# Performance work log

Measured on AMD Instinct MI355X. Metric: run time of the kernel, lower is better.

The kernel has to match this reference:

```python
import jax, jax.numpy as jnp
import numpy as np
from functools import partial

VOCAB = 32000
EMBED = 512
HIDDEN = 1024
NUM_LAYERS = 2
REP_PENALTY = 1.2
BATCH, SEQ = 64, 128


def _lstm_layer(xs, w_ih, w_hh, b_ih, b_hh):
    """PyTorch-convention LSTM layer. xs: [B,T,D_in] -> hs: [B,T,H].
    Gate order i,f,g,o; weights [4H, D_in]/[4H, H]."""
    B = xs.shape[0]
    H = w_hh.shape[1]
    # precompute input projections for all timesteps: [B,T,4H]
    x_proj = jnp.einsum('btd,gd->btg', xs, w_ih) + b_ih + b_hh

    def step(carry, xp):
        h, c = carry
        gates = xp + h @ w_hh.T  # [B,4H]
        i, f, g, o = jnp.split(gates, 4, axis=-1)
        i = jax.nn.sigmoid(i)
        f = jax.nn.sigmoid(f)
        g = jnp.tanh(g)
        o = jax.nn.sigmoid(o)
        c = f * c + i * g
        h = o * jnp.tanh(c)
        return (h, c), h

    h0 = jnp.zeros((B, H), xs.dtype)
    c0 = jnp.zeros((B, H), xs.dtype)
    _, hs = jax.lax.scan(step, (h0, c0), x_proj.transpose(1, 0, 2))  # [T,B,H]
    return hs.transpose(1, 0, 2)


def setup_inputs() -> dict:
    key = jax.random.key(0)
    ks = jax.random.split(key, 16)
    s_emb = 1.0  # nn.Embedding default init ~ N(0,1)
    x = jax.random.randint(ks[0], (BATCH, SEQ), 0, VOCAB, dtype=jnp.int32)
    emb = jax.random.normal(ks[1], (VOCAB, EMBED), jnp.float32) * s_emb

    def lstm_params(k, d_in):
        k1, k2, k3, k4 = jax.random.split(k, 4)
        s = 1.0 / np.sqrt(HIDDEN)
        return (
            jax.random.uniform(k1, (4 * HIDDEN, d_in), jnp.float32, -s, s),
            jax.random.uniform(k2, (4 * HIDDEN, HIDDEN), jnp.float32, -s, s),
            jax.random.uniform(k3, (4 * HIDDEN,), jnp.float32, -s, s),
            jax.random.uniform(k4, (4 * HIDDEN,), jnp.float32, -s, s),
        )

    w_ih0, w_hh0, b_ih0, b_hh0 = lstm_params(ks[2], EMBED)
    w_ih1, w_hh1, b_ih1, b_hh1 = lstm_params(ks[3], HIDDEN)
    s_fc = 1.0 / np.sqrt(HIDDEN)
    fc_w = jax.random.uniform(ks[4], (VOCAB, HIDDEN), jnp.float32, -s_fc, s_fc)
    fc_b = jax.random.uniform(ks[5], (VOCAB,), jnp.float32, -s_fc, s_fc)
    return {
        'x': x, 'emb': emb,
        'w_ih0': w_ih0, 'w_hh0': w_hh0, 'b_ih0': b_ih0, 'b_hh0': b_hh0,
        'w_ih1': w_ih1, 'w_hh1': w_hh1, 'b_ih1': b_ih1, 'b_hh1': b_hh1,
        'fc_w': fc_w, 'fc_b': fc_b,
    }


def reference(x, emb, w_ih0, w_hh0, b_ih0, b_hh0,
              w_ih1, w_hh1, b_ih1, b_hh1, fc_w, fc_b):
    h = emb[x]                                          # [B,S,E] embedding lookup
    h = _lstm_layer(h, w_ih0, w_hh0, b_ih0, b_hh0)      # [B,S,H]
    h = _lstm_layer(h, w_ih1, w_hh1, b_ih1, b_hh1)      # [B,S,H]
    last = h[:, -1, :]                                  # [B,H]
    out = last @ fc_w.T + fc_b                          # [B,V]
    # repetition penalty: each occurrence of token t in row i divides out[i,t]
    # by the penalty once => out[i,t] /= penalty**count(t in x[i]).
    B = x.shape[0]
    rows = jnp.broadcast_to(jnp.arange(B)[:, None], x.shape)
    counts = jnp.zeros((B, VOCAB), out.dtype).at[rows, x].add(1.0)
    out = out / jnp.power(jnp.asarray(REP_PENALTY, out.dtype), counts)
    return out
```

## Files before the change

kernel.cpp:

```cpp
#include <hip/hip_runtime.h>
#include <hip/hip_bf16.h>
#include <stdint.h>

#define NB 64
#define NT 128
#define NE 512
#define NH 1024
#define NV 32000
#define NM (NB*NT)

#define NWG 256
#define NTH 512
#define FLAG_STRIDE 32u

#define HSLOT_B (NB*NH*2u)
#define WS_FLAGS   0u
#define WS_FLAG_B  (NWG*FLAG_STRIDE*4u)
#define WS_H0      WS_FLAG_B
#define WS_H1      (WS_H0 + 129u*HSLOT_B)
#define WS_CNT     (WS_H1 + 129u*HSLOT_B)
#define WS_XS0     (WS_CNT + 4u*NB*NV)
#define WS_NEEDED  (WS_XS0 + 2u*NM*NE)

typedef __attribute__((ext_vector_type(8))) short bf16x8;
typedef __attribute__((ext_vector_type(4))) float f32x4;

__device__ __forceinline__ unsigned short f2bf(float f) {
  unsigned u = __float_as_uint(f);
  u += 0x7FFFu + ((u >> 16) & 1u);
  return (unsigned short)(u >> 16);
}
__device__ __forceinline__ float sigmoidf_(float x) {
  return 1.0f / (1.0f + expf(-x));
}
__device__ __forceinline__ bf16x8 pack8(float4 a, float4 b) {
  bf16x8 v;
  v[0]=(short)f2bf(a.x); v[1]=(short)f2bf(a.y); v[2]=(short)f2bf(a.z); v[3]=(short)f2bf(a.w);
  v[4]=(short)f2bf(b.x); v[5]=(short)f2bf(b.y); v[6]=(short)f2bf(b.z); v[7]=(short)f2bf(b.w);
  return v;
}

__device__ __forceinline__ void gbar_light(unsigned* flags, unsigned n) {
  __syncthreads();
  if (threadIdx.x == 0)
    __hip_atomic_store(&flags[(unsigned)blockIdx.x * FLAG_STRIDE], n,
                       __ATOMIC_RELAXED, __HIP_MEMORY_SCOPE_AGENT);
  if (threadIdx.x < NWG) {
    while (__hip_atomic_load(&flags[(unsigned)threadIdx.x * FLAG_STRIDE],
                             __ATOMIC_RELAXED, __HIP_MEMORY_SCOPE_AGENT) < n)
      __builtin_amdgcn_s_sleep(8);
  }
  __syncthreads();
}

#define MFMA(a,b,c) __builtin_amdgcn_mfma_f32_16x16x32_bf16((a),(b),(c),0,0,0)

__global__ void __launch_bounds__(NTH, 2)
lstm_all(const int* __restrict__ x, const float* __restrict__ emb,
         const float* __restrict__ w_ih0, const float* __restrict__ w_hh0,
         const float* __restrict__ b_ih0, const float* __restrict__ b_hh0,
         const float* __restrict__ w_ih1, const float* __restrict__ w_hh1,
         const float* __restrict__ b_ih1, const float* __restrict__ b_hh1,
         const float* __restrict__ fc_w, const float* __restrict__ fc_b,
         float* __restrict__ out, unsigned char* __restrict__ wsb)
{
  __shared__ unsigned short sWih1[32*64*8];
  __shared__ unsigned short sWih0[16*64*8];
  __shared__ float sG0[NB][16], sG1a[NB][16], sG1b[NB][16], sGih[NB][16];
  __shared__ float sB0[16], sB1[16];
  __shared__ alignas(8) unsigned short sH0[NB][4], sH1[NB][4];

  const int wg  = blockIdx.x;
  const int tid = threadIdx.x;
  const int wave = tid >> 6, lane = tid & 63;
  const int lr = lane & 15, lq = lane >> 4;

  unsigned* flags = (unsigned*)(wsb + WS_FLAGS);
  unsigned short* hist0 = (unsigned short*)(wsb + WS_H0);
  unsigned short* hist1 = (unsigned short*)(wsb + WS_H1);
  unsigned* counts = (unsigned*)(wsb + WS_CNT);
  unsigned short* xs0 = (unsigned short*)(wsb + WS_XS0);

  const int gr = (lr >> 2)*NH + wg*4 + (lr & 3);

  const unsigned kkw = (unsigned)wg >> 3, lqw = ((unsigned)wg >> 1) & 3, j0 = ((unsigned)wg & 1)*4;
  const size_t pubOff = ((size_t)((lane>>4)*32 + kkw)*64 + lqw*16 + (lane&15))*8 + j0;

  bf16x8 breg[32];
  {
    const float* wsrc = (wave < 4 ? w_hh0 : w_hh1) + (size_t)gr*NH + lq*8;
    #pragma unroll
    for (int kk = 0; kk < 32; ++kk)
      breg[kk] = pack8(*(const float4*)(wsrc + kk*32), *(const float4*)(wsrc + kk*32 + 4));
  }

  for (int i = wg*NTH + tid; i < NM*(NE/8); i += NWG*NTH) {
    int m = i >> 6;
    int e8 = (i & 63) << 3;
    int t = m >> 6, b = m & 63;
    int tok = x[b*NT + t];
    const float* s = emb + (size_t)tok*NE + e8;
    union { bf16x8 v8; unsigned long long u[2]; } u;
    u.v8 = pack8(*(const float4*)s, *(const float4*)(s + 4));
    int mblk = m >> 4, lrm = m & 15;
    int kk = e8 >> 5, lqm = (e8 >> 3) & 3;
    size_t elem = ((size_t)(mblk*16 + kk)*64 + lqm*16 + lrm) * 8;
    unsigned long long* dst = (unsigned long long*)(xs0 + elem);
    __hip_atomic_store(dst,   u.u[0], __ATOMIC_RELAXED, __HIP_MEMORY_SCOPE_AGENT);
    __hip_atomic_store(dst+1, u.u[1], __ATOMIC_RELAXED, __HIP_MEMORY_SCOPE_AGENT);
  }

  for (int i = tid; i < 32*64; i += NTH) {
    int kk = i >> 6, l = i & 63;
    int glr = l & 15, glq = l >> 4;
    int ggr = (glr >> 2)*NH + wg*4 + (glr & 3);
    const float* p = w_ih1 + (size_t)ggr*NH + kk*32 + glq*8;
    ((bf16x8*)sWih1)[i] = pack8(*(const float4*)p, *(const float4*)(p + 4));
  }
  for (int i = tid; i < 16*64; i += NTH) {
    int kk = i >> 6, l = i & 63;
    int glr = l & 15, glq = l >> 4;
    int ggr = (glr >> 2)*NH + wg*4 + (glr & 3);
    const float* p = w_ih0 + (size_t)ggr*NE + kk*32 + glq*8;
    ((bf16x8*)sWih0)[i] = pack8(*(const float4*)p, *(const float4*)(p + 4));
  }
  if (tid < 16) {
    int g2 = (tid >> 2)*NH + wg*4 + (tid & 3);
    sB0[tid] = b_ih0[g2] + b_hh0[g2];
    sB1[tid] = b_ih1[g2] + b_hh1[g2];
  }
  {
    int i = wg*NTH + tid;
    if (i < NB*NT) {
      int b = i >> 7;
      atomicAdd(&counts[(size_t)b*NV + x[i]], 1u);
    }
  }
  unsigned bar = 1;
  gbar_light(flags, bar);

  float c_reg = 0.f;
  const int cb = (tid & 255) >> 2, cu = tid & 3;
  for (int t = 0; t <= NT; ++t) {
    if (wave < 4) {
      const unsigned short* A = hist0 + (size_t)t*(NB*NH) + (size_t)(wave*2048 + lane)*8;
      f32x4 a0 = {0.f,0.f,0.f,0.f}, a1 = {0.f,0.f,0.f,0.f};
      #pragma unroll
      for (int kk = 0; kk < 32; ++kk) {
        bf16x8 af = *(const bf16x8*)(A + kk*512);
        a0 = MFMA(af, breg[kk], a0);
        a1 = MFMA(af, ((const bf16x8*)sWih1)[kk*64 + lane], a1);
      }
      #pragma unroll
      for (int r = 0; r < 4; ++r) {
        sG0 [wave*16 + lq*4 + r][lr] = a0[r];
        sG1a[wave*16 + lq*4 + r][lr] = a1[r];
      }
    } else {
      if (t >= 1) {
        const unsigned short* A = hist1 + (size_t)(t-1)*(NB*NH) + (size_t)((wave-4)*2048 + lane)*8;
        f32x4 a2 = {0.f,0.f,0.f,0.f};
        #pragma unroll
        for (int kk = 0; kk < 32; ++kk)
          a2 = MFMA(*(const bf16x8*)(A + kk*512), breg[kk], a2);
        #pragma unroll
        for (int r = 0; r < 4; ++r) sG1b[(wave-4)*16 + lq*4 + r][lr] = a2[r];
      }
      if (t < NT) {
        const unsigned short* A = xs0 + ((size_t)(t*4 + (wave-4))*1024 + lane)*8;
        f32x4 ai = {0.f,0.f,0.f,0.f};
        #pragma unroll
        for (int kk = 0; kk < 16; ++kk)
          ai = MFMA(*(const bf16x8*)(A + kk*512), ((const bf16x8*)sWih0)[kk*64 + lane], ai);
        #pragma unroll
        for (int r = 0; r < 4; ++r) sGih[(wave-4)*16 + lq*4 + r][lr] = ai[r];
      }
    }
    __syncthreads();
    if (tid < 256) {
      if (t < NT) {
        float gi = sG0[cb][cu]    + sGih[cb][cu]    + sB0[cu];
        float gf = sG0[cb][4+cu]  + sGih[cb][4+cu]  + sB0[4+cu];
        float gg = sG0[cb][8+cu]  + sGih[cb][8+cu]  + sB0[8+cu];
        float go = sG0[cb][12+cu] + sGih[cb][12+cu] + sB0[12+cu];
        float ii = sigmoidf_(gi), ff = sigmoidf_(gf), g = tanhf(gg), oo = sigmoidf_(go);
        c_reg = ff*c_reg + ii*g;
        sH0[cb][cu] = f2bf(oo * tanhf(c_reg));
      }
    } else {
      if (t >= 1) {
        float gi = sG1a[cb][cu]    + sG1b[cb][cu]    + sB1[cu];
        float gf = sG1a[cb][4+cu]  + sG1b[cb][4+cu]  + sB1[4+cu];
        float gg = sG1a[cb][8+cu]  + sG1b[cb][8+cu]  + sB1[8+cu];
        float go = sG1a[cb][12+cu] + sG1b[cb][12+cu] + sB1[12+cu];
        float ii = sigmoidf_(gi), ff = sigmoidf_(gf), g = tanhf(gg), oo = sigmoidf_(go);
        c_reg = ff*c_reg + ii*g;
        sH1[cb][cu] = f2bf(oo * tanhf(c_reg));
      }
    }
    __syncthreads();
    if (wave == 0 && t < NT) {
      unsigned long long v = *(const unsigned long long*)&sH0[lane][0];
      __hip_atomic_store((unsigned long long*)(hist0 + (size_t)(t+1)*(NB*NH) + pubOff),
                         v, __ATOMIC_RELAXED, __HIP_MEMORY_SCOPE_AGENT);
    }
    if (wave == 1 && t >= 1) {
      unsigned long long v = *(const unsigned long long*)&sH1[lane][0];
      __hip_atomic_store((unsigned long long*)(hist1 + (size_t)t*(NB*NH) + pubOff),
                         v, __ATOMIC_RELAXED, __HIP_MEMORY_SCOPE_AGENT);
    }
    gbar_light(flags, ++bar);
  }

  {
    const unsigned short* ab = hist1 + (size_t)128*(NB*NH) + (size_t)lane*8;
    int tile = wg*8 + wave;
    if (tile < NV/16) {
      int c0 = tile*16;
      const float* wb = fc_w + (size_t)(c0 + lr)*NH + lq*8;
      f32x4 acc[4] = {{0.f,0.f,0.f,0.f},{0.f,0.f,0.f,0.f},{0.f,0.f,0.f,0.f},{0.f,0.f,0.f,0.f}};
      #pragma unroll 4
      for (int kk = 0; kk < 32; ++kk) {
        bf16x8 bfv = pack8(*(const float4*)(wb + kk*32), *(const float4*)(wb + kk*32 + 4));
        #pragma unroll
        for (int mt = 0; mt < 4; ++mt) {
          bf16x8 af = *(const bf16x8*)(ab + (size_t)(mt*32 + kk)*512);
          acc[mt] = MFMA(af, bfv, acc[mt]);
        }
      }
      int c = c0 + lr;
      float fb = fc_b[c];
      #pragma unroll
      for (int mt = 0; mt < 4; ++mt) {
        #pragma unroll
        for (int r = 0; r < 4; ++r) {
          int b = mt*16 + lq*4 + r;
          unsigned cnt = counts[(size_t)b*NV + c];
          float v = (acc[mt][r] + fb) * exp2f(-0.26303440583379378f * (float)cnt);
          out[(size_t)b*NV + c] = v;
        }
      }
    }
  }
}

extern "C" void kernel_launch(void* const* d_in, const int* in_sizes, int n_in,
                              void* d_out, int out_size, void* d_ws, size_t ws_size,
                              hipStream_t stream) {
  const int*   x     = (const int*)  d_in[0];
  const float* emb   = (const float*)d_in[1];
  const float* w_ih0 = (const float*)d_in[2];
  const float* w_hh0 = (const float*)d_in[3];
  const float* b_ih0 = (const float*)d_in[4];
  const float* b_hh0 = (const float*)d_in[5];
  const float* w_ih1 = (const float*)d_in[6];
  const float* w_hh1 = (const float*)d_in[7];
  const float* b_ih1 = (const float*)d_in[8];
  const float* b_hh1 = (const float*)d_in[9];
  const float* fc_w  = (const float*)d_in[10];
  const float* fc_b  = (const float*)d_in[11];
  if (ws_size < WS_NEEDED) return;
  unsigned char* ws = (unsigned char*)d_ws;
  hipMemsetAsync(ws + WS_FLAGS, 0, WS_FLAG_B, stream);
  hipMemsetAsync(ws + WS_H0, 0, HSLOT_B, stream);
  hipMemsetAsync(ws + WS_H1, 0, HSLOT_B, stream);
  hipMemsetAsync(ws + WS_CNT, 0, 4u*NB*NV, stream);
  hipLaunchKernelGGL(lstm_all, dim3(NWG), dim3(NTH), 0, stream,
                     x, emb, w_ih0, w_hh0, b_ih0, b_hh0,
                     w_ih1, w_hh1, b_ih1, b_hh1, fc_w, fc_b,
                     (float*)d_out, (unsigned char*)d_ws);
}
```

Before: 998.9 us.

## Decouple LSTM layer waves with per-wave flags and LDS counters instead of grid barriers

Replaces the lock-step per-timestep grid barrier with separate global flag arrays for layer 0 and layer 1. Each wave polls only the 64 workgroups whose outputs it consumes, and waves inside a workgroup coordinate through LDS atomic counters. Layer-0 waves now also compute the input projection, and a 4-deep LDS ring buffers the layer-1 input-projection partials, so layer 1 can trail layer 0 in a wavefront pipeline instead of sharing one barrier. The goal is to remove full-grid barrier latency and idle time on the serial recurrence. In exchange the hand-rolled memory ordering (relaxed stores, manual waitcnt and fence macros, spin loops) is harder to reason about and could deadlock or race.

```diff
diff --git a/kernel.cpp b/kernel.cpp
--- a/kernel.cpp
+++ b/kernel.cpp
@@ -8,15 +8,17 @@
 #define NH 1024
 #define NV 32000
 #define NM (NB*NT)
+#define NBNH (NB*NH)
 
 #define NWG 256
 #define NTH 512
 #define FLAG_STRIDE 32u
 
 #define HSLOT_B (NB*NH*2u)
-#define WS_FLAGS   0u
-#define WS_FLAG_B  (NWG*FLAG_STRIDE*4u)
-#define WS_H0      WS_FLAG_B
+#define WS_FLAGS_S 0u
+#define WS_FLAGS_A (32u*1024u)
+#define WS_FLAGS_B (64u*1024u)
+#define WS_H0      (96u*1024u)
 #define WS_H1      (WS_H0 + 129u*HSLOT_B)
 #define WS_CNT     (WS_H1 + 129u*HSLOT_B)
 #define WS_XS0     (WS_CNT + 4u*NB*NV)
@@ -24,6 +26,13 @@
 
 typedef __attribute__((ext_vector_type(8))) short bf16x8;
 typedef __attribute__((ext_vector_type(4))) float f32x4;
+
+#define SCOPE_WG  __HIP_MEMORY_SCOPE_WORKGROUP
+#define SCOPE_AG  __HIP_MEMORY_SCOPE_AGENT
+
+#define FENCE() do { asm volatile("" ::: "memory"); __builtin_amdgcn_sched_barrier(0); } while (0)
+#define LGKM0() do { asm volatile("s_waitcnt lgkmcnt(0)" ::: "memory"); __builtin_amdgcn_sched_barrier(0); } while (0)
+#define VM0()   do { asm volatile("s_waitcnt vmcnt(0)" ::: "memory"); __builtin_amdgcn_sched_barrier(0); } while (0)
 
 __device__ __forceinline__ unsigned short f2bf(float f) {
   unsigned u = __float_as_uint(f);
@@ -43,11 +52,9 @@
 __device__ __forceinline__ void gbar_light(unsigned* flags, unsigned n) {
   __syncthreads();
   if (threadIdx.x == 0)
-    __hip_atomic_store(&flags[(unsigned)blockIdx.x * FLAG_STRIDE], n,
-                       __ATOMIC_RELAXED, __HIP_MEMORY_SCOPE_AGENT);
+    __hip_atomic_store(&flags[(unsigned)blockIdx.x * FLAG_STRIDE], n, __ATOMIC_RELAXED, SCOPE_AG);
   if (threadIdx.x < NWG) {
-    while (__hip_atomic_load(&flags[(unsigned)threadIdx.x * FLAG_STRIDE],
-                             __ATOMIC_RELAXED, __HIP_MEMORY_SCOPE_AGENT) < n)
+    while (__hip_atomic_load(&flags[(unsigned)threadIdx.x * FLAG_STRIDE], __ATOMIC_RELAXED, SCOPE_AG) < n)
       __builtin_amdgcn_s_sleep(8);
   }
   __syncthreads();
@@ -66,16 +73,20 @@
 {
   __shared__ unsigned short sWih1[32*64*8];
   __shared__ unsigned short sWih0[16*64*8];
-  __shared__ float sG0[NB][16], sG1a[NB][16], sG1b[NB][16], sGih[NB][16];
+  __shared__ float sG0[NB][16], sGih[NB][16], sG1b[NB][16];
+  __shared__ float ringP[4][NB][16];
   __shared__ float sB0[16], sB1[16];
   __shared__ alignas(8) unsigned short sH0[NB][4], sH1[NB][4];
+  __shared__ unsigned ldsCnt[12];
 
   const int wg  = blockIdx.x;
   const int tid = threadIdx.x;
   const int wave = tid >> 6, lane = tid & 63;
   const int lr = lane & 15, lq = lane >> 4;
 
-  unsigned* flags = (unsigned*)(wsb + WS_FLAGS);
+  unsigned* flagsS = (unsigned*)(wsb + WS_FLAGS_S);
+  unsigned* flagsA = (unsigned*)(wsb + WS_FLAGS_A);
+  unsigned* flagsB = (unsigned*)(wsb + WS_FLAGS_B);
   unsigned short* hist0 = (unsigned short*)(wsb + WS_H0);
   unsigned short* hist1 = (unsigned short*)(wsb + WS_H1);
   unsigned* counts = (unsigned*)(wsb + WS_CNT);
@@ -84,7 +95,8 @@
   const int gr = (lr >> 2)*NH + wg*4 + (lr & 3);
 
   const unsigned kkw = (unsigned)wg >> 3, lqw = ((unsigned)wg >> 1) & 3, j0 = ((unsigned)wg & 1)*4;
-  const size_t pubOff = ((size_t)((lane>>4)*32 + kkw)*64 + lqw*16 + (lane&15))*8 + j0;
+
+  if (tid < 12) ldsCnt[tid] = 0;
 
   bf16x8 breg[32];
   {
@@ -106,8 +118,8 @@
     int kk = e8 >> 5, lqm = (e8 >> 3) & 3;
     size_t elem = ((size_t)(mblk*16 + kk)*64 + lqm*16 + lrm) * 8;
     unsigned long long* dst = (unsigned long long*)(xs0 + elem);
-    __hip_atomic_store(dst,   u.u[0], __ATOMIC_RELAXED, __HIP_MEMORY_SCOPE_AGENT);
-    __hip_atomic_store(dst+1, u.u[1], __ATOMIC_RELAXED, __HIP_MEMORY_SCOPE_AGENT);
+    __hip_atomic_store(dst,   u.u[0], __ATOMIC_RELAXED, SCOPE_AG);
+    __hip_atomic_store(dst+1, u.u[1], __ATOMIC_RELAXED, SCOPE_AG);
   }
 
   for (int i = tid; i < 32*64; i += NTH) {
@@ -136,84 +148,150 @@
       atomicAdd(&counts[(size_t)b*NV + x[i]], 1u);
     }
   }
-  unsigned bar = 1;
-  gbar_light(flags, bar);
-
-  float c_reg = 0.f;
-  const int cb = (tid & 255) >> 2, cu = tid & 3;
-  for (int t = 0; t <= NT; ++t) {
-    if (wave < 4) {
-      const unsigned short* A = hist0 + (size_t)t*(NB*NH) + (size_t)(wave*2048 + lane)*8;
-      f32x4 a0 = {0.f,0.f,0.f,0.f}, a1 = {0.f,0.f,0.f,0.f};
-      #pragma unroll
-      for (int kk = 0; kk < 32; ++kk) {
-        bf16x8 af = *(const bf16x8*)(A + kk*512);
-        a0 = MFMA(af, breg[kk], a0);
-        a1 = MFMA(af, ((const bf16x8*)sWih1)[kk*64 + lane], a1);
-      }
-      #pragma unroll
-      for (int r = 0; r < 4; ++r) {
-        sG0 [wave*16 + lq*4 + r][lr] = a0[r];
-        sG1a[wave*16 + lq*4 + r][lr] = a1[r];
-      }
-    } else {
-      if (t >= 1) {
-        const unsigned short* A = hist1 + (size_t)(t-1)*(NB*NH) + (size_t)((wave-4)*2048 + lane)*8;
-        f32x4 a2 = {0.f,0.f,0.f,0.f};
+  gbar_light(flagsS, 1);
+
+  const int cbl = lane >> 2, cu = lane & 3;
+
+  if (wave < 4) {
+    const int w = wave;
+    const size_t pubOffW = ((size_t)(w*32 + kkw)*64 + lqw*16 + lane)*8 + j0;
+    float c0 = 0.f;
+    for (int t = 0; t <= NT; ++t) {
+      while (__hip_atomic_load(&flagsA[(unsigned)(w*64 + lane)*FLAG_STRIDE],
+                               __ATOMIC_RELAXED, SCOPE_AG) < (unsigned)t)
+        __builtin_amdgcn_s_sleep(1);
+      if (lane == 0) {
+        __hip_atomic_fetch_add(&ldsCnt[10], 1u, __ATOMIC_ACQ_REL, SCOPE_WG);
+        while (__hip_atomic_load(&ldsCnt[10], __ATOMIC_ACQUIRE, SCOPE_WG) < 4u*(unsigned)(t+1)) {}
+      }
+      FENCE();
+      if (t >= 4) {
+        if (lane == 0)
+          while (__hip_atomic_load(&ldsCnt[4+w], __ATOMIC_ACQUIRE, SCOPE_WG) < (unsigned)(t-3)) {}
+        FENCE();
+      }
+      const unsigned short* A = hist0 + (size_t)t*NBNH + (size_t)(w*2048 + lane)*8;
+      f32x4 a0 = {0.f,0.f,0.f,0.f}, a1 = {0.f,0.f,0.f,0.f}, ai = {0.f,0.f,0.f,0.f};
+      if (t < NT) {
+        #pragma unroll
+        for (int kk = 0; kk < 32; ++kk) {
+          bf16x8 af = *(const bf16x8*)(A + kk*512);
+          a0 = MFMA(af, breg[kk], a0);
+          a1 = MFMA(af, ((const bf16x8*)sWih1)[kk*64 + lane], a1);
+        }
+        const unsigned short* X = xs0 + ((size_t)(t*4 + w)*1024 + lane)*8;
+        #pragma unroll
+        for (int kk = 0; kk < 16; ++kk)
+          ai = MFMA(*(const bf16x8*)(X + kk*512), ((const bf16x8*)sWih0)[kk*64 + lane], ai);
+      } else {
         #pragma unroll
         for (int kk = 0; kk < 32; ++kk)
-          a2 = MFMA(*(const bf16x8*)(A + kk*512), breg[kk], a2);
-        #pragma unroll
-        for (int r = 0; r < 4; ++r) sG1b[(wave-4)*16 + lq*4 + r][lr] = a2[r];
+          a1 = MFMA(*(const bf16x8*)(A + kk*512), ((const bf16x8*)sWih1)[kk*64 + lane], a1);
+      }
+      {
+        int rs = t & 3;
+        #pragma unroll
+        for (int r = 0; r < 4; ++r) ringP[rs][w*16 + lq*4 + r][lr] = a1[r];
       }
       if (t < NT) {
-        const unsigned short* A = xs0 + ((size_t)(t*4 + (wave-4))*1024 + lane)*8;
-        f32x4 ai = {0.f,0.f,0.f,0.f};
-        #pragma unroll
-        for (int kk = 0; kk < 16; ++kk)
-          ai = MFMA(*(const bf16x8*)(A + kk*512), ((const bf16x8*)sWih0)[kk*64 + lane], ai);
-        #pragma unroll
-        for (int r = 0; r < 4; ++r) sGih[(wave-4)*16 + lq*4 + r][lr] = ai[r];
-      }
-    }
-    __syncthreads();
-    if (tid < 256) {
+        #pragma unroll
+        for (int r = 0; r < 4; ++r) {
+          sG0 [w*16 + lq*4 + r][lr] = a0[r];
+          sGih[w*16 + lq*4 + r][lr] = ai[r];
+        }
+      }
+      LGKM0();
+      if (lane == 0)
+        __hip_atomic_fetch_add(&ldsCnt[w], 1u, __ATOMIC_RELEASE, SCOPE_WG);
       if (t < NT) {
+        int cb = w*16 + cbl;
         float gi = sG0[cb][cu]    + sGih[cb][cu]    + sB0[cu];
         float gf = sG0[cb][4+cu]  + sGih[cb][4+cu]  + sB0[4+cu];
         float gg = sG0[cb][8+cu]  + sGih[cb][8+cu]  + sB0[8+cu];
         float go = sG0[cb][12+cu] + sGih[cb][12+cu] + sB0[12+cu];
         float ii = sigmoidf_(gi), ff = sigmoidf_(gf), g = tanhf(gg), oo = sigmoidf_(go);
-        c_reg = ff*c_reg + ii*g;
-        sH0[cb][cu] = f2bf(oo * tanhf(c_reg));
-      }
-    } else {
-      if (t >= 1) {
-        float gi = sG1a[cb][cu]    + sG1b[cb][cu]    + sB1[cu];
-        float gf = sG1a[cb][4+cu]  + sG1b[cb][4+cu]  + sB1[4+cu];
-        float gg = sG1a[cb][8+cu]  + sG1b[cb][8+cu]  + sB1[8+cu];
-        float go = sG1a[cb][12+cu] + sG1b[cb][12+cu] + sB1[12+cu];
+        c0 = ff*c0 + ii*g;
+        sH0[cb][cu] = f2bf(oo * tanhf(c0));
+        LGKM0();
+        if (lane < 16) {
+          unsigned long long v = *(const unsigned long long*)&sH0[w*16 + lane][0];
+          __hip_atomic_store((unsigned long long*)(hist0 + (size_t)(t+1)*NBNH + pubOffW),
+                             v, __ATOMIC_RELAXED, SCOPE_AG);
+        }
+        VM0();
+        if (lane == 0)
+          __hip_atomic_fetch_add(&ldsCnt[8], 1u, __ATOMIC_RELEASE, SCOPE_WG);
+        if (w == 0 && lane == 0) {
+          while (__hip_atomic_load(&ldsCnt[8], __ATOMIC_ACQUIRE, SCOPE_WG) < 4u*(unsigned)(t+1)) {}
+          __hip_atomic_store(&flagsA[(unsigned)wg*FLAG_STRIDE], (unsigned)(t+1),
+                             __ATOMIC_RELAXED, SCOPE_AG);
+        }
+      }
+    }
+  } else {
+    const int w1 = wave - 4;
+    const size_t pubOffW = ((size_t)(w1*32 + kkw)*64 + lqw*16 + lane)*8 + j0;
+    float c1 = 0.f;
+    for (int s = 0; s < NT; ++s) {
+      while (__hip_atomic_load(&flagsB[(unsigned)(w1*64 + lane)*FLAG_STRIDE],
+                               __ATOMIC_RELAXED, SCOPE_AG) < (unsigned)s)
+        __builtin_amdgcn_s_sleep(1);
+      if (lane == 0) {
+        __hip_atomic_fetch_add(&ldsCnt[11], 1u, __ATOMIC_ACQ_REL, SCOPE_WG);
+        while (__hip_atomic_load(&ldsCnt[11], __ATOMIC_ACQUIRE, SCOPE_WG) < 4u*(unsigned)(s+1)) {}
+      }
+      FENCE();
+      if (lane == 0)
+        while (__hip_atomic_load(&ldsCnt[w1], __ATOMIC_ACQUIRE, SCOPE_WG) < (unsigned)(s+2)) {}
+      FENCE();
+      const unsigned short* A = hist1 + (size_t)s*NBNH + (size_t)(w1*2048 + lane)*8;
+      f32x4 a2 = {0.f,0.f,0.f,0.f};
+      #pragma unroll
+      for (int kk = 0; kk < 32; ++kk)
+        a2 = MFMA(*(const bf16x8*)(A + kk*512), breg[kk], a2);
+      #pragma unroll
+      for (int r = 0; r < 4; ++r) sG1b[w1*16 + lq*4 + r][lr] = a2[r];
+      LGKM0();
+      {
+        int cb = w1*16 + cbl;
+        int rs = (s+1) & 3;
+        float gi = ringP[rs][cb][cu]    + sG1b[cb][cu]    + sB1[cu];
+        float gf = ringP[rs][cb][4+cu]  + sG1b[cb][4+cu]  + sB1[4+cu];
+        float gg = ringP[rs][cb][8+cu]  + sG1b[cb][8+cu]  + sB1[8+cu];
+        float go = ringP[rs][cb][12+cu] + sG1b[cb][12+cu] + sB1[12+cu];
         float ii = sigmoidf_(gi), ff = sigmoidf_(gf), g = tanhf(gg), oo = sigmoidf_(go);
-        c_reg = ff*c_reg + ii*g;
-        sH1[cb][cu] = f2bf(oo * tanhf(c_reg));
+        c1 = ff*c1 + ii*g;
+        sH1[cb][cu] = f2bf(oo * tanhf(c1));
+      }
+      if (lane == 0)
+        __hip_atomic_fetch_add(&ldsCnt[4+w1], 1u, __ATOMIC_RELEASE, SCOPE_WG);
+      LGKM0();
+      if (lane < 16) {
+        unsigned long long v = *(const unsigned long long*)&sH1[w1*16 + lane][0];
+        __hip_atomic_store((unsigned long long*)(hist1 + (size_t)(s+1)*NBNH + pubOffW),
+                           v, __ATOMIC_RELAXED, SCOPE_AG);
+      }
+      VM0();
+      if (lane == 0)
+        __hip_atomic_fetch_add(&ldsCnt[9], 1u, __ATOMIC_RELEASE, SCOPE_WG);
+      if (w1 == 0 && lane == 0) {
+        while (__hip_atomic_load(&ldsCnt[9], __ATOMIC_ACQUIRE, SCOPE_WG) < 4u*(unsigned)(s+1)) {}
+        __hip_atomic_store(&flagsB[(unsigned)wg*FLAG_STRIDE], (unsigned)(s+1),
+                           __ATOMIC_RELAXED, SCOPE_AG);
       }
     }
-    __syncthreads();
-    if (wave == 0 && t < NT) {
-      unsigned long long v = *(const unsigned long long*)&sH0[lane][0];
-      __hip_atomic_store((unsigned long long*)(hist0 + (size_t)(t+1)*(NB*NH) + pubOff),
-                         v, __ATOMIC_RELAXED, __HIP_MEMORY_SCOPE_AGENT);
-    }
-    if (wave == 1 && t >= 1) {
-      unsigned long long v = *(const unsigned long long*)&sH1[lane][0];
-      __hip_atomic_store((unsigned long long*)(hist1 + (size_t)t*(NB*NH) + pubOff),
-                         v, __ATOMIC_RELAXED, __HIP_MEMORY_SCOPE_AGENT);
-    }
-    gbar_light(flags, ++bar);
-  }
+  }
+
+  __syncthreads();
+  if (tid < NWG) {
+    while (__hip_atomic_load(&flagsB[(unsigned)tid*FLAG_STRIDE], __ATOMIC_RELAXED, SCOPE_AG)
+           < (unsigned)NT)
+      __builtin_amdgcn_s_sleep(4);
+  }
+  __syncthreads();
 
   {
-    const unsigned short* ab = hist1 + (size_t)128*(NB*NH) + (size_t)lane*8;
+    const unsigned short* ab = hist1 + (size_t)128*NBNH + (size_t)lane*8;
     int tile = wg*8 + wave;
     if (tile < NV/16) {
       int c0 = tile*16;
@@ -261,7 +339,7 @@
   const float* fc_b  = (const float*)d_in[11];
   if (ws_size < WS_NEEDED) return;
   unsigned char* ws = (unsigned char*)d_ws;
-  hipMemsetAsync(ws + WS_FLAGS, 0, WS_FLAG_B, stream);
+  hipMemsetAsync(ws, 0, WS_H0, stream);
   hipMemsetAsync(ws + WS_H0, 0, HSLOT_B, stream);
   hipMemsetAsync(ws + WS_H1, 0, HSLOT_B, stream);
   hipMemsetAsync(ws + WS_CNT, 0, 4u*NB*NV, stream);
```

Result: slower. 1.343 ms (+34.4%).

## Replace per-step global barrier with split per-layer flag counters

Applied to the files above, without the earlier changes.

Replaces the single grid-wide barrier per timestep with separate layer-0 and layer-1 progress flags. Each workgroup waits only on the flags its next step depends on, and each wave publishes its own h slice with a workgroup-local counter that raises the flag once all four waves are done. This removes one block-wide sync and lets the two layers drift apart instead of marching in lockstep. The cost is more spin-polling traffic and subtle memory-ordering requirements around relaxed stores and waitcnt-based fences.

```diff
diff --git a/kernel.cpp b/kernel.cpp
--- a/kernel.cpp
+++ b/kernel.cpp
@@ -8,15 +8,17 @@
 #define NH 1024
 #define NV 32000
 #define NM (NB*NT)
+#define NBNH (NB*NH)
 
 #define NWG 256
 #define NTH 512
 #define FLAG_STRIDE 32u
 
 #define HSLOT_B (NB*NH*2u)
-#define WS_FLAGS   0u
-#define WS_FLAG_B  (NWG*FLAG_STRIDE*4u)
-#define WS_H0      WS_FLAG_B
+#define WS_FLAGS_S 0u
+#define WS_FLAGS_A (32u*1024u)
+#define WS_FLAGS_B (64u*1024u)
+#define WS_H0      (96u*1024u)
 #define WS_H1      (WS_H0 + 129u*HSLOT_B)
 #define WS_CNT     (WS_H1 + 129u*HSLOT_B)
 #define WS_XS0     (WS_CNT + 4u*NB*NV)
@@ -24,6 +26,12 @@
 
 typedef __attribute__((ext_vector_type(8))) short bf16x8;
 typedef __attribute__((ext_vector_type(4))) float f32x4;
+
+#define SCOPE_WG  __HIP_MEMORY_SCOPE_WORKGROUP
+#define SCOPE_AG  __HIP_MEMORY_SCOPE_AGENT
+
+#define LGKM0() do { asm volatile("s_waitcnt lgkmcnt(0)" ::: "memory"); __builtin_amdgcn_sched_barrier(0); } while (0)
+#define VM0()   do { asm volatile("s_waitcnt vmcnt(0)" ::: "memory"); __builtin_amdgcn_sched_barrier(0); } while (0)
 
 __device__ __forceinline__ unsigned short f2bf(float f) {
   unsigned u = __float_as_uint(f);
@@ -43,11 +51,9 @@
 __device__ __forceinline__ void gbar_light(unsigned* flags, unsigned n) {
   __syncthreads();
   if (threadIdx.x == 0)
-    __hip_atomic_store(&flags[(unsigned)blockIdx.x * FLAG_STRIDE], n,
-                       __ATOMIC_RELAXED, __HIP_MEMORY_SCOPE_AGENT);
+    __hip_atomic_store(&flags[(unsigned)blockIdx.x * FLAG_STRIDE], n, __ATOMIC_RELAXED, SCOPE_AG);
   if (threadIdx.x < NWG) {
-    while (__hip_atomic_load(&flags[(unsigned)threadIdx.x * FLAG_STRIDE],
-                             __ATOMIC_RELAXED, __HIP_MEMORY_SCOPE_AGENT) < n)
+    while (__hip_atomic_load(&flags[(unsigned)threadIdx.x * FLAG_STRIDE], __ATOMIC_RELAXED, SCOPE_AG) < n)
       __builtin_amdgcn_s_sleep(8);
   }
   __syncthreads();
@@ -66,16 +72,19 @@
 {
   __shared__ unsigned short sWih1[32*64*8];
   __shared__ unsigned short sWih0[16*64*8];
-  __shared__ float sG0[NB][16], sG1a[NB][16], sG1b[NB][16], sGih[NB][16];
+  __shared__ float sG0[NB][16], sGih[NB][16], sG1a[NB][16], sG1b[NB][16];
   __shared__ float sB0[16], sB1[16];
   __shared__ alignas(8) unsigned short sH0[NB][4], sH1[NB][4];
+  __shared__ unsigned cntA, cntB;
 
   const int wg  = blockIdx.x;
   const int tid = threadIdx.x;
   const int wave = tid >> 6, lane = tid & 63;
   const int lr = lane & 15, lq = lane >> 4;
 
-  unsigned* flags = (unsigned*)(wsb + WS_FLAGS);
+  unsigned* flagsS = (unsigned*)(wsb + WS_FLAGS_S);
+  unsigned* flagsA = (unsigned*)(wsb + WS_FLAGS_A);
+  unsigned* flagsB = (unsigned*)(wsb + WS_FLAGS_B);
   unsigned short* hist0 = (unsigned short*)(wsb + WS_H0);
   unsigned short* hist1 = (unsigned short*)(wsb + WS_H1);
   unsigned* counts = (unsigned*)(wsb + WS_CNT);
@@ -84,7 +93,10 @@
   const int gr = (lr >> 2)*NH + wg*4 + (lr & 3);
 
   const unsigned kkw = (unsigned)wg >> 3, lqw = ((unsigned)wg >> 1) & 3, j0 = ((unsigned)wg & 1)*4;
-  const size_t pubOff = ((size_t)((lane>>4)*32 + kkw)*64 + lqw*16 + (lane&15))*8 + j0;
+  const unsigned rbw = (unsigned)(wave & 3);
+  const size_t pubOff = ((size_t)(rbw*32 + kkw)*64 + lqw*16 + lane)*8 + j0;
+
+  if (tid == 0) { cntA = 0; cntB = 0; }
 
   bf16x8 breg[32];
   {
@@ -106,8 +118,8 @@
     int kk = e8 >> 5, lqm = (e8 >> 3) & 3;
     size_t elem = ((size_t)(mblk*16 + kk)*64 + lqm*16 + lrm) * 8;
     unsigned long long* dst = (unsigned long long*)(xs0 + elem);
-    __hip_atomic_store(dst,   u.u[0], __ATOMIC_RELAXED, __HIP_MEMORY_SCOPE_AGENT);
-    __hip_atomic_store(dst+1, u.u[1], __ATOMIC_RELAXED, __HIP_MEMORY_SCOPE_AGENT);
+    __hip_atomic_store(dst,   u.u[0], __ATOMIC_RELAXED, SCOPE_AG);
+    __hip_atomic_store(dst+1, u.u[1], __ATOMIC_RELAXED, SCOPE_AG);
   }
 
   for (int i = tid; i < 32*64; i += NTH) {
@@ -136,29 +148,57 @@
       atomicAdd(&counts[(size_t)b*NV + x[i]], 1u);
     }
   }
-  unsigned bar = 1;
-  gbar_light(flags, bar);
+  gbar_light(flagsS, 1);
 
   float c_reg = 0.f;
   const int cb = (tid & 255) >> 2, cu = tid & 3;
   for (int t = 0; t <= NT; ++t) {
+    if (tid < NWG) {
+      while (__hip_atomic_load(&flagsA[(unsigned)tid * FLAG_STRIDE],
+                               __ATOMIC_RELAXED, SCOPE_AG) < (unsigned)t)
+        __builtin_amdgcn_s_sleep(2);
+    } else {
+      unsigned need = (t > 0) ? (unsigned)(t - 1) : 0u;
+      while (__hip_atomic_load(&flagsB[(unsigned)(tid - NWG) * FLAG_STRIDE],
+                               __ATOMIC_RELAXED, SCOPE_AG) < need)
+        __builtin_amdgcn_s_sleep(2);
+    }
+    __syncthreads();
+
     if (wave < 4) {
-      const unsigned short* A = hist0 + (size_t)t*(NB*NH) + (size_t)(wave*2048 + lane)*8;
+      const unsigned short* A = hist0 + (size_t)t*NBNH + (size_t)(wave*2048 + lane)*8;
       f32x4 a0 = {0.f,0.f,0.f,0.f}, a1 = {0.f,0.f,0.f,0.f};
-      #pragma unroll
-      for (int kk = 0; kk < 32; ++kk) {
-        bf16x8 af = *(const bf16x8*)(A + kk*512);
-        a0 = MFMA(af, breg[kk], a0);
-        a1 = MFMA(af, ((const bf16x8*)sWih1)[kk*64 + lane], a1);
-      }
-      #pragma unroll
-      for (int r = 0; r < 4; ++r) {
-        sG0 [wave*16 + lq*4 + r][lr] = a0[r];
-        sG1a[wave*16 + lq*4 + r][lr] = a1[r];
+      if (t < NT) {
+        #pragma unroll
+        for (int kk = 0; kk < 32; ++kk) {
+          bf16x8 af = *(const bf16x8*)(A + kk*512);
+          a0 = MFMA(af, breg[kk], a0);
+          a1 = MFMA(af, ((const bf16x8*)sWih1)[kk*64 + lane], a1);
+        }
+        #pragma unroll
+        for (int r = 0; r < 4; ++r) {
+          sG0 [wave*16 + lq*4 + r][lr] = a0[r];
+          sG1a[wave*16 + lq*4 + r][lr] = a1[r];
+        }
+      } else {
+        #pragma unroll
+        for (int kk = 0; kk < 32; ++kk)
+          a1 = MFMA(*(const bf16x8*)(A + kk*512), ((const bf16x8*)sWih1)[kk*64 + lane], a1);
+        #pragma unroll
+        for (int r = 0; r < 4; ++r) sG1a[wave*16 + lq*4 + r][lr] = a1[r];
       }
     } else {
+      if (t < NT) {
+        const unsigned short* X = xs0 + ((size_t)(t*4 + (wave-4))*1024 + lane)*8;
+        f32x4 ai = {0.f,0.f,0.f,0.f};
+        #pragma unroll
+        for (int kk = 0; kk < 16; ++kk)
+          ai = MFMA(*(const bf16x8*)(X + kk*512), ((const bf16x8*)sWih0)[kk*64 + lane], ai);
+        #pragma unroll
+        for (int r = 0; r < 4; ++r) sGih[(wave-4)*16 + lq*4 + r][lr] = ai[r];
+      }
       if (t >= 1) {
-        const unsigned short* A = hist1 + (size_t)(t-1)*(NB*NH) + (size_t)((wave-4)*2048 + lane)*8;
+        const unsigned short* A = hist1 + (size_t)(t-1)*NBNH + (size_t)((wave-4)*2048 + lane)*8;
         f32x4 a2 = {0.f,0.f,0.f,0.f};
         #pragma unroll
         for (int kk = 0; kk < 32; ++kk)
@@ -166,18 +206,10 @@
         #pragma unroll
         for (int r = 0; r < 4; ++r) sG1b[(wave-4)*16 + lq*4 + r][lr] = a2[r];
       }
-      if (t < NT) {
-        const unsigned short* A = xs0 + ((size_t)(t*4 + (wave-4))*1024 + lane)*8;
-        f32x4 ai = {0.f,0.f,0.f,0.f};
-        #pragma unroll
-        for (int kk = 0; kk < 16; ++kk)
-          ai = MFMA(*(const bf16x8*)(A + kk*512), ((const bf16x8*)sWih0)[kk*64 + lane], ai);
-        #pragma unroll
-        for (int r = 0; r < 4; ++r) sGih[(wave-4)*16 + lq*4 + r][lr] = ai[r];
-      }
     }
     __syncthreads();
-    if (tid < 256) {
+
+    if (wave < 4) {
       if (t < NT) {
         float gi = sG0[cb][cu]    + sGih[cb][cu]    + sB0[cu];
         float gf = sG0[cb][4+cu]  + sGih[cb][4+cu]  + sB0[4+cu];
@@ -186,6 +218,19 @@
         float ii = sigmoidf_(gi), ff = sigmoidf_(gf), g = tanhf(gg), oo = sigmoidf_(go);
         c_reg = ff*c_reg + ii*g;
         sH0[cb][cu] = f2bf(oo * tanhf(c_reg));
+        LGKM0();
+        if (lane < 16) {
+          unsigned long long v = *(const unsigned long long*)&sH0[(wave&3)*16 + lane][0];
+          __hip_atomic_store((unsigned long long*)(hist0 + (size_t)(t+1)*NBNH + pubOff),
+                             v, __ATOMIC_RELAXED, SCOPE_AG);
+        }
+        VM0();
+        if (lane == 0) {
+          unsigned old = __hip_atomic_fetch_add(&cntA, 1u, __ATOMIC_ACQ_REL, SCOPE_WG);
+          if (old == 4u*(unsigned)(t+1) - 1u)
+            __hip_atomic_store(&flagsA[(unsigned)wg * FLAG_STRIDE], (unsigned)(t+1),
+                               __ATOMIC_RELAXED, SCOPE_AG);
+        }
       }
     } else {
       if (t >= 1) {
@@ -196,24 +241,32 @@
         float ii = sigmoidf_(gi), ff = sigmoidf_(gf), g = tanhf(gg), oo = sigmoidf_(go);
         c_reg = ff*c_reg + ii*g;
         sH1[cb][cu] = f2bf(oo * tanhf(c_reg));
-      }
-    }
-    __syncthreads();
-    if (wave == 0 && t < NT) {
-      unsigned long long v = *(const unsigned long long*)&sH0[lane][0];
-      __hip_atomic_store((unsigned long long*)(hist0 + (size_t)(t+1)*(NB*NH) + pubOff),
-                         v, __ATOMIC_RELAXED, __HIP_MEMORY_SCOPE_AGENT);
-    }
-    if (wave == 1 && t >= 1) {
-      unsigned long long v = *(const unsigned long long*)&sH1[lane][0];
-      __hip_atomic_store((unsigned long long*)(hist1 + (size_t)t*(NB*NH) + pubOff),
-                         v, __ATOMIC_RELAXED, __HIP_MEMORY_SCOPE_AGENT);
-    }
-    gbar_light(flags, ++bar);
-  }
+        LGKM0();
+        if (lane < 16) {
+          unsigned long long v = *(const unsigned long long*)&sH1[(wave&3)*16 + lane][0];
+          __hip_atomic_store((unsigned long long*)(hist1 + (size_t)t*NBNH + pubOff),
+                             v, __ATOMIC_RELAXED, SCOPE_AG);
+        }
+        VM0();
+        if (lane == 0) {
+          unsigned old = __hip_atomic_fetch_add(&cntB, 1u, __ATOMIC_ACQ_REL, SCOPE_WG);
+          if (old == 4u*(unsigned)t - 1u)
+            __hip_atomic_store(&flagsB[(unsigned)wg * FLAG_STRIDE], (unsigned)t,
+                               __ATOMIC_RELAXED, SCOPE_AG);
+        }
+      }
+    }
+  }
+
+  if (tid >= NWG) {
+    while (__hip_atomic_load(&flagsB[(unsigned)(tid - NWG) * FLAG_STRIDE],
+                             __ATOMIC_RELAXED, SCOPE_AG) < (unsigned)NT)
+      __builtin_amdgcn_s_sleep(4);
+  }
+  __syncthreads();
 
   {
-    const unsigned short* ab = hist1 + (size_t)128*(NB*NH) + (size_t)lane*8;
+    const unsigned short* ab = hist1 + (size_t)128*NBNH + (size_t)lane*8;
     int tile = wg*8 + wave;
     if (tile < NV/16) {
       int c0 = tile*16;
@@ -261,7 +314,7 @@
   const float* fc_b  = (const float*)d_in[11];
   if (ws_size < WS_NEEDED) return;
   unsigned char* ws = (unsigned char*)d_ws;
-  hipMemsetAsync(ws + WS_FLAGS, 0, WS_FLAG_B, stream);
+  hipMemsetAsync(ws, 0, WS_H0, stream);
   hipMemsetAsync(ws + WS_H0, 0, HSLOT_B, stream);
   hipMemsetAsync(ws + WS_H1, 0, HSLOT_B, stream);
   hipMemsetAsync(ws + WS_CNT, 0, 4u*NB*NV, stream);
```

New measurement: 1.254 ms. +25.5%, slower.
